# Performance work log

Hardware: AMD Instinct MI355X
Metric: run time of the kernel (lower is better)

## Reference

```python
import jax, jax.numpy as jnp
import numpy as np

D_MODEL = 1024
N_HEADS = 16
HEAD_DIM = D_MODEL // N_HEADS
SEQ_LEN = 2048
D_FF = 4 * D_MODEL
LCC_SCALE = 0.1
LN_EPS = 1e-5
NORM_EPS = 1e-12  # F.normalize eps


def _layer_norm(x, g, b):
    mu = jnp.mean(x, axis=-1, keepdims=True)
    var = jnp.mean(jnp.square(x - mu), axis=-1, keepdims=True)
    return (x - mu) * jax.lax.rsqrt(var + LN_EPS) * g + b


def setup_inputs() -> dict:
    key = jax.random.key(0)
    ks = jax.random.split(key, 8)
    s = 0.02  # weight init scale
    return {
        "x": jax.random.normal(ks[0], (SEQ_LEN, D_MODEL), jnp.float32),
        "lcc_values": jax.random.uniform(ks[1], (SEQ_LEN,), jnp.float32),
        "w_qkv": jax.random.normal(ks[2], (D_MODEL, 3 * D_MODEL), jnp.float32) * s,
        "b_qkv": jnp.zeros((3 * D_MODEL,), jnp.float32),
        "w_out": jax.random.normal(ks[3], (D_MODEL, D_MODEL), jnp.float32) * s,
        "b_out": jnp.zeros((D_MODEL,), jnp.float32),
        "ln1_g": jnp.ones((D_MODEL,), jnp.float32),
        "ln1_b": jnp.zeros((D_MODEL,), jnp.float32),
        "ln2_g": jnp.ones((D_MODEL,), jnp.float32),
        "ln2_b": jnp.zeros((D_MODEL,), jnp.float32),
        "w_ff1": jax.random.normal(ks[4], (D_MODEL, D_FF), jnp.float32) * s,
        "b_ff1": jnp.zeros((D_FF,), jnp.float32),
        "w_ff2": jax.random.normal(ks[5], (D_FF, D_MODEL), jnp.float32) * s,
        "b_ff2": jnp.zeros((D_MODEL,), jnp.float32),
    }


def reference(x, lcc_values, w_qkv, b_qkv, w_out, b_out, ln1_g, ln1_b,
              ln2_g, ln2_b, w_ff1, b_ff1, w_ff2, b_ff2):
    L = x.shape[0]
    scaling = HEAD_DIM ** -0.5

    normed = _layer_norm(x, ln1_g, ln1_b)
    qkv = normed @ w_qkv + b_qkv                      # [L, 3D]
    qkv = qkv.reshape(L, 3, N_HEADS, HEAD_DIM)
    q = jnp.transpose(qkv[:, 0], (1, 0, 2))           # [H, L, d]
    k = jnp.transpose(qkv[:, 1], (1, 0, 2))
    v = jnp.transpose(qkv[:, 2], (1, 0, 2))

    # cosine attention: L2-normalize q, k
    q = q / jnp.maximum(jnp.linalg.norm(q, axis=-1, keepdims=True), NORM_EPS)
    k = k / jnp.maximum(jnp.linalg.norm(k, axis=-1, keepdims=True), NORM_EPS)
    q = q * scaling

    scores = jnp.einsum('hld,hmd->hlm', q, k)         # [H, L, L]
    bias = (lcc_values[:, None] + lcc_values[None, :]) * 0.5 * LCC_SCALE
    scores = jnp.clip(scores + bias[None], -10.0, 10.0)
    probs = jax.nn.softmax(scores, axis=-1)

    attn = jnp.einsum('hlm,hmd->hld', probs, v)       # [H, L, d]
    attn = jnp.transpose(attn, (1, 0, 2)).reshape(L, D_MODEL)
    x = x + (attn @ w_out + b_out)

    normed2 = _layer_norm(x, ln2_g, ln2_b)
    h = jax.nn.gelu(normed2 @ w_ff1 + b_ff1, approximate=False)
    x = x + (h @ w_ff2 + b_ff2)
    return x
```

## Files before the change

### kernel.cpp

```cpp
#include <hip/hip_runtime.h>
#include <hip/hip_bf16.h>

#define D_MODEL 1024
#define SEQ 2048
#define NH 16
#define HD 64
#define DFF 4096

typedef __attribute__((ext_vector_type(8))) __bf16 bf16x8;
typedef __attribute__((ext_vector_type(4))) float f32x4;

__device__ __forceinline__ unsigned short f2bf(float f) {
    union { float f; unsigned u; } v; v.f = f;
    unsigned r = v.u + 0x7fffu + ((v.u >> 16) & 1u);
    return (unsigned short)(r >> 16);
}
__device__ __forceinline__ unsigned pack2(float a, float b) {
    return (unsigned)f2bf(a) | ((unsigned)f2bf(b) << 16);
}
__device__ __forceinline__ float bf2f(unsigned short u) {
    union { unsigned u; float f; } v; v.u = ((unsigned)u) << 16;
    return v.f;
}
__device__ __forceinline__ bf16x8 ld_frag(const unsigned short* p) {
    union { uint4 u; bf16x8 b; } c;
    c.u = *(const uint4*)p;
    return c.b;
}

typedef __attribute__((address_space(3))) unsigned lds_u32;
typedef const __attribute__((address_space(1))) unsigned glob_u32;
__device__ __forceinline__ void gl_lds16(const unsigned short* g, unsigned short* l) {
    __builtin_amdgcn_global_load_lds((glob_u32*)g, (lds_u32*)l, 16, 0, 0);
}

#define MFMA16(a,b,c) __builtin_amdgcn_mfma_f32_16x16x32_bf16(a,b,c,0,0,0)

__global__ __launch_bounds__(256) void wcast_all(const float* __restrict__ wq, const float* __restrict__ wo,
                                                 const float* __restrict__ wf1, const float* __restrict__ wf2,
                                                 unsigned short* __restrict__ oq, unsigned short* __restrict__ oo,
                                                 unsigned short* __restrict__ of1, unsigned short* __restrict__ of2) {
    __shared__ unsigned short lt[64][72];
    int id = blockIdx.x;
    const float* W; unsigned short* O; int K, N, nb, kb;
    if (id < 768)       { W = wq;  O = oq;  K = 1024; N = 3072; nb = id % 48; kb = id / 48; }
    else if (id < 1024) { id -= 768;  W = wo;  O = oo;  K = 1024; N = 1024; nb = id & 15; kb = id >> 4; }
    else if (id < 2048) { id -= 1024; W = wf1; O = of1; K = 1024; N = 4096; nb = id & 63; kb = id >> 6; }
    else                { id -= 2048; W = wf2; O = of2; K = 4096; N = 1024; nb = id & 15; kb = id >> 4; }
    int t = threadIdx.x;
    int r = t >> 2, c0 = (t & 3) << 4;
    const float* src = W + (size_t)(kb*64 + r) * N + nb*64 + c0;
    float4 f0 = ((const float4*)src)[0];
    float4 f1 = ((const float4*)src)[1];
    float4 f2 = ((const float4*)src)[2];
    float4 f3 = ((const float4*)src)[3];
    unsigned* dst = (unsigned*)&lt[r][c0];
    dst[0]=pack2(f0.x,f0.y); dst[1]=pack2(f0.z,f0.w);
    dst[2]=pack2(f1.x,f1.y); dst[3]=pack2(f1.z,f1.w);
    dst[4]=pack2(f2.x,f2.y); dst[5]=pack2(f2.z,f2.w);
    dst[6]=pack2(f3.x,f3.y); dst[7]=pack2(f3.z,f3.w);
    __syncthreads();
    int n_ = t >> 2, k0 = (t & 3) << 4;
    unsigned obuf[8];
#pragma unroll
    for (int i = 0; i < 8; i++)
        obuf[i] = (unsigned)lt[k0 + 2*i][n_] | ((unsigned)lt[k0 + 2*i + 1][n_] << 16);
    unsigned short* out = O + (size_t)(nb*64 + n_) * K + kb*64 + k0;
    ((uint4*)out)[0] = *(uint4*)&obuf[0];
    ((uint4*)out)[1] = *(uint4*)&obuf[4];
}

__global__ __launch_bounds__(256) void ln_kernel(const float* __restrict__ x,
                                                 const float* __restrict__ g,
                                                 const float* __restrict__ b,
                                                 unsigned short* __restrict__ out) {
    int row = blockIdx.x, t = threadIdx.x;
    float4 v = ((const float4*)(x + (size_t)row * D_MODEL))[t];
    float s  = v.x + v.y + v.z + v.w;
    float sq = v.x*v.x + v.y*v.y + v.z*v.z + v.w*v.w;
#pragma unroll
    for (int m = 1; m < 64; m <<= 1) { s += __shfl_xor(s, m, 64); sq += __shfl_xor(sq, m, 64); }
    __shared__ float ls[4], lq[4];
    int wave = t >> 6, lane = t & 63;
    if (lane == 0) { ls[wave] = s; lq[wave] = sq; }
    __syncthreads();
    s  = ls[0]+ls[1]+ls[2]+ls[3];
    sq = lq[0]+lq[1]+lq[2]+lq[3];
    float mu  = s * (1.0f / D_MODEL);
    float var = sq * (1.0f / D_MODEL) - mu * mu;
    float rs  = rsqrtf(var + 1e-5f);
    int c = t * 4;
    float y0 = (v.x - mu) * rs * g[c+0] + b[c+0];
    float y1 = (v.y - mu) * rs * g[c+1] + b[c+1];
    float y2 = (v.z - mu) * rs * g[c+2] + b[c+2];
    float y3 = (v.w - mu) * rs * g[c+3] + b[c+3];
    unsigned* o = (unsigned*)(out + (size_t)row * D_MODEL + c);
    o[0] = pack2(y0, y1); o[1] = pack2(y2, y3);
}

__global__ __launch_bounds__(256) void reduce_ln(const float* __restrict__ x,
                                                 const float* __restrict__ bout,
                                                 const unsigned short* __restrict__ parts,
                                                 const float* __restrict__ g,
                                                 const float* __restrict__ b,
                                                 float* __restrict__ x1,
                                                 unsigned short* __restrict__ x2n) {
    int row = blockIdx.x, t = threadIdx.x;
    int i = row * 256 + t;
    float4 v = ((const float4*)x)[i];
    float4 bb = ((const float4*)bout)[t];
    v.x += bb.x; v.y += bb.y; v.z += bb.z; v.w += bb.w;
    ushort4 u0 = ((const ushort4*)parts)[i];
    ushort4 u1 = ((const ushort4*)(parts + (size_t)SEQ*D_MODEL))[i];
    v.x += bf2f(u0.x) + bf2f(u1.x);
    v.y += bf2f(u0.y) + bf2f(u1.y);
    v.z += bf2f(u0.z) + bf2f(u1.z);
    v.w += bf2f(u0.w) + bf2f(u1.w);
    ((float4*)x1)[i] = v;
    float s  = v.x + v.y + v.z + v.w;
    float sq = v.x*v.x + v.y*v.y + v.z*v.z + v.w*v.w;
#pragma unroll
    for (int m = 1; m < 64; m <<= 1) { s += __shfl_xor(s, m, 64); sq += __shfl_xor(sq, m, 64); }
    __shared__ float ls[4], lq[4];
    int wave = t >> 6, lane = t & 63;
    if (lane == 0) { ls[wave] = s; lq[wave] = sq; }
    __syncthreads();
    s  = ls[0]+ls[1]+ls[2]+ls[3];
    sq = lq[0]+lq[1]+lq[2]+lq[3];
    float mu  = s * (1.0f / D_MODEL);
    float var = sq * (1.0f / D_MODEL) - mu * mu;
    float rs  = rsqrtf(var + 1e-5f);
    int c = t * 4;
    float y0 = (v.x - mu) * rs * g[c+0] + b[c+0];
    float y1 = (v.y - mu) * rs * g[c+1] + b[c+1];
    float y2 = (v.z - mu) * rs * g[c+2] + b[c+2];
    float y3 = (v.w - mu) * rs * g[c+3] + b[c+3];
    unsigned* o = (unsigned*)(x2n + (size_t)row * D_MODEL + c);
    o[0] = pack2(y0, y1); o[1] = pack2(y2, y3);
}

__global__ __launch_bounds__(256) void reduce_ff2(const float* __restrict__ res,
                                                  const float* __restrict__ bias,
                                                  const unsigned short* __restrict__ parts,
                                                  float* __restrict__ out) {
    int i = blockIdx.x * 256 + threadIdx.x;
    float4 r = ((const float4*)res)[i];
    float4 b = ((const float4*)bias)[i & (D_MODEL/4 - 1)];
    r.x += b.x; r.y += b.y; r.z += b.z; r.w += b.w;
#pragma unroll
    for (int p = 0; p < 4; p++) {
        ushort4 u = ((const ushort4*)(parts + (size_t)p * SEQ * D_MODEL))[i];
        r.x += bf2f(u.x); r.y += bf2f(u.y); r.z += bf2f(u.z); r.w += bf2f(u.w);
    }
    ((float4*)out)[i] = r;
}

#define TMg 128
#define TNg 128
#define BKq 32
#define BUF_U16 ((TMg + TNg) * BKq)
#define SMEM_U16 (4 * BUF_U16)
__device__ __forceinline__ void gemm_core(const unsigned short* __restrict__ A,
                                          const unsigned short* __restrict__ Bt,
                                          int K, int K0, int KS, int bm, int bn,
                                          unsigned short* smem, f32x4 acc[4][4],
                                          int wave, int lane) {
    int quad = lane >> 4, lr = lane & 15;
    const unsigned short* pa[2]; const unsigned short* pb[2];
    int aoff[2], boff[2];
#pragma unroll
    for (int i = 0; i < 2; i++) {
        int rl = i*64 + wave*16 + (lane >> 2);
        int sc = (lane & 3) ^ (rl & 3);
        pa[i] = A + (size_t)(bm*TMg + rl) * K + K0 + sc*8;
        pb[i] = Bt + (size_t)(bn*TNg + rl) * K + K0 + sc*8;
        aoff[i] = (i*64 + wave*16) * BKq;
        boff[i] = TMg*BKq + (i*64 + wave*16) * BKq;
    }
    int wr = (wave >> 1) * 64, wc = (wave & 1) * 64;
    int foA[4], foB[4];
#pragma unroll
    for (int i = 0; i < 4; i++) {
        int ra = wr + i*16 + lr;
        foA[i] = ra*BKq + (quad ^ (ra & 3))*8;
        int rb = wc + i*16 + lr;
        foB[i] = TMg*BKq + rb*BKq + (quad ^ (rb & 3))*8;
    }
    int T = KS >> 5;
#pragma unroll
    for (int t = 0; t < 3; t++) {
        unsigned short* s = smem + t * BUF_U16;
#pragma unroll
        for (int i = 0; i < 2; i++) {
            gl_lds16(pa[i] + t*BKq, s + aoff[i]);
            gl_lds16(pb[i] + t*BKq, s + boff[i]);
        }
    }
    for (int t = 0; t < T; t++) {
        if (t < T - 2)      asm volatile("s_waitcnt vmcnt(8)" ::: "memory");
        else if (t == T - 2) asm volatile("s_waitcnt vmcnt(4)" ::: "memory");
        else                 asm volatile("s_waitcnt vmcnt(0)" ::: "memory");
        __builtin_amdgcn_s_barrier();
        if (t + 3 < T) {
            unsigned short* s = smem + ((t + 3) & 3) * BUF_U16;
#pragma unroll
            for (int i = 0; i < 2; i++) {
                gl_lds16(pa[i] + (t+3)*BKq, s + aoff[i]);
                gl_lds16(pb[i] + (t+3)*BKq, s + boff[i]);
            }
        }
        const unsigned short* s = smem + (t & 3) * BUF_U16;
        bf16x8 af[4], bfr[4];
#pragma unroll
        for (int i = 0; i < 4; i++) af[i] = ld_frag(s + foA[i]);
#pragma unroll
        for (int j = 0; j < 4; j++) bfr[j] = ld_frag(s + foB[j]);
        __builtin_amdgcn_s_setprio(1);
#pragma unroll
        for (int i = 0; i < 4; i++)
#pragma unroll
            for (int j = 0; j < 4; j++)
                acc[i][j] = MFMA16(af[i], bfr[j], acc[i][j]);
        __builtin_amdgcn_s_setprio(0);
    }
}

__device__ __forceinline__ void acc_init(f32x4 acc[4][4]) {
    f32x4 z = {0.f, 0.f, 0.f, 0.f};
#pragma unroll
    for (int i = 0; i < 4; i++)
#pragma unroll
        for (int j = 0; j < 4; j++) acc[i][j] = z;
}

__global__ __launch_bounds__(256) void k_gemm_qkv(const unsigned short* __restrict__ A,
                                                  const unsigned short* __restrict__ Bt,
                                                  const float* __restrict__ bias,
                                                  unsigned short* __restrict__ qn,
                                                  unsigned short* __restrict__ kn,
                                                  unsigned short* __restrict__ vt) {
    __shared__ unsigned short smem[SMEM_U16];
    int t = threadIdx.x;
    int bn = blockIdx.x, bm = blockIdx.y;
    int wave = t >> 6, lane = t & 63;
    int quad = lane >> 4, lr = lane & 15;
    f32x4 acc[4][4];
    acc_init(acc);
    gemm_core(A, Bt, 1024, 0, 1024, bm, bn, smem, acc, wave, lane);

    int wr = (wave >> 1) * 64, wc = (wave & 1) * 64;
    int sec = bn >> 3, hp = bn & 7;
    float bv[4];
#pragma unroll
    for (int j = 0; j < 4; j++) bv[j] = bias[bn*TNg + wc + j*16 + lr];
#pragma unroll
    for (int i = 0; i < 4; i++)
#pragma unroll
        for (int j = 0; j < 4; j++)
#pragma unroll
            for (int r = 0; r < 4; r++) acc[i][j][r] += bv[j];

    if (sec < 2) {
        int h = hp*2 + (wave & 1);
        unsigned short* dst = (sec == 0) ? qn : kn;
        float mul = (sec == 0) ? 0.125f : 1.0f;
#pragma unroll
        for (int i = 0; i < 4; i++)
#pragma unroll
            for (int r = 0; r < 4; r++) {
                float ss = 0.f;
#pragma unroll
                for (int j = 0; j < 4; j++) ss += acc[i][j][r]*acc[i][j][r];
                ss += __shfl_xor(ss, 1, 64); ss += __shfl_xor(ss, 2, 64);
                ss += __shfl_xor(ss, 4, 64); ss += __shfl_xor(ss, 8, 64);
                float scale = mul / fmaxf(sqrtf(ss), 1e-12f);
                int row = bm*TMg + wr + i*16 + quad*4 + r;
                size_t base = ((size_t)h*SEQ + row) * HD;
#pragma unroll
                for (int j = 0; j < 4; j++)
                    dst[base + j*16 + lr] = f2bf(acc[i][j][r] * scale);
            }
    } else {
        __syncthreads();
        unsigned short (*lv)[136] = (unsigned short (*)[136])smem;
#pragma unroll
        for (int i = 0; i < 4; i++)
#pragma unroll
            for (int j = 0; j < 4; j++)
#pragma unroll
                for (int r = 0; r < 4; r++)
                    lv[wc + j*16 + lr][wr + i*16 + quad*4 + r] = f2bf(acc[i][j][r]);
        __syncthreads();
        int d = t >> 1, l0 = (t & 1) * 64;
        unsigned short* ov = vt + ((size_t)(hp*128 + d)) * SEQ + bm*TMg + l0;
#pragma unroll
        for (int c = 0; c < 8; c++)
            ((uint4*)ov)[c] = *(uint4*)&lv[d][l0 + c*8];
    }
}

template<int SPLITK>
__device__ __forceinline__ void gemm_part(const unsigned short* A, const unsigned short* Bt,
                                          unsigned short* C, int M, int N, int K) {
    __shared__ unsigned short smem[SMEM_U16];
    int t = threadIdx.x;
    int bn = blockIdx.x, bm = blockIdx.y, kz = blockIdx.z;
    int wave = t >> 6, lane = t & 63;
    int quad = lane >> 4, lr = lane & 15;
    int KS = K / SPLITK;
    f32x4 acc[4][4];
    acc_init(acc);
    gemm_core(A, Bt, K, kz*KS, KS, bm, bn, smem, acc, wave, lane);
    int wr = (wave >> 1) * 64, wc = (wave & 1) * 64;
    unsigned short* P = C + (size_t)kz * M * N;
#pragma unroll
    for (int i = 0; i < 4; i++)
#pragma unroll
        for (int j = 0; j < 4; j++) {
            int row0 = bm*TMg + wr + i*16 + quad*4;
            int col  = bn*TNg + wc + j*16 + lr;
#pragma unroll
            for (int r = 0; r < 4; r++)
                P[(size_t)(row0 + r) * N + col] = f2bf(acc[i][j][r]);
        }
}
__global__ __launch_bounds__(256) void k_gemm_op(const unsigned short* A, const unsigned short* Bt,
                                                 unsigned short* C, int M, int N, int K) {
    gemm_part<2>(A, Bt, C, M, N, K);
}
__global__ __launch_bounds__(256) void k_gemm_ff2(const unsigned short* A, const unsigned short* Bt,
                                                  unsigned short* C, int M, int N, int K) {
    gemm_part<4>(A, Bt, C, M, N, K);
}

__global__ __launch_bounds__(256) void k_gemm_ff1(const unsigned short* __restrict__ A,
                                                  const unsigned short* __restrict__ Bt,
                                                  const float* __restrict__ bias,
                                                  unsigned short* __restrict__ C,
                                                  int M, int N, int K) {
    __shared__ unsigned short smem[SMEM_U16];
    int t = threadIdx.x;
    int bn = blockIdx.x, bm = blockIdx.y;
    int wave = t >> 6, lane = t & 63;
    int quad = lane >> 4, lr = lane & 15;
    f32x4 acc[4][4];
    acc_init(acc);
    gemm_core(A, Bt, K, 0, K, bm, bn, smem, acc, wave, lane);
    int wr = (wave >> 1) * 64, wc = (wave & 1) * 64;
#pragma unroll
    for (int i = 0; i < 4; i++)
#pragma unroll
        for (int j = 0; j < 4; j++) {
            int row0 = bm*TMg + wr + i*16 + quad*4;
            int col  = bn*TNg + wc + j*16 + lr;
            float bvv = bias[col];
#pragma unroll
            for (int r = 0; r < 4; r++) {
                float v = acc[i][j][r] + bvv;
                v = 0.5f * v * (1.0f + erff(v * 0.70710678118654752f));
                C[(size_t)(row0 + r) * N + col] = f2bf(v);
            }
        }
}

#define KSPLIT 2
#define KTILES (SEQ / 64 / KSPLIT)
__global__ __launch_bounds__(256) void attn_kernel(const unsigned short* __restrict__ qn,
                                                   const unsigned short* __restrict__ kn,
                                                   const unsigned short* __restrict__ vt,
                                                   const float* __restrict__ lcc,
                                                   float* __restrict__ num_ws,
                                                   float* __restrict__ den_ws) {
    __shared__ unsigned short lQP[64*64];
    __shared__ unsigned short lK[2][64*64];
    __shared__ unsigned short lV[2][64*64];
    int h = blockIdx.x, qb = blockIdx.y, kz = blockIdx.z;
    int t = threadIdx.x;
    int wave = t >> 6, lane = t & 63, quad = lane >> 4, lr = lane & 15;
    int r0 = lane >> 3;
    int ch = lane & 7;

    const unsigned short* kn0 = kn + (size_t)h*SEQ*HD + (size_t)kz*(SEQ/KSPLIT)*HD;
    const unsigned short* vt0 = vt + (size_t)h*HD*SEQ + kz*(SEQ/KSPLIT);
    const float* lcc0 = lcc + kz*(SEQ/KSPLIT);

#pragma unroll
    for (int i = 0; i < 2; i++) {
        int rl = wave*16 + i*8 + r0;
        int ss = ch ^ (rl & 7);
        gl_lds16(qn + ((size_t)h*SEQ + qb*64 + rl)*HD + ss*8, lQP + (wave*16 + i*8)*64);
        gl_lds16(kn0 + (size_t)rl*HD + ss*8,                  lK[0] + (wave*16 + i*8)*64);
        gl_lds16(vt0 + (size_t)rl*SEQ + ss*8,                 lV[0] + (wave*16 + i*8)*64);
    }
    __syncthreads();

    bf16x8 aq0 = ld_frag(lQP + (wave*16 + lr)*64 + ((quad     ^ (lr & 7)))*8);
    bf16x8 aq1 = ld_frag(lQP + (wave*16 + lr)*64 + (((quad+4) ^ (lr & 7)))*8);

    f32x4 z = {0.f, 0.f, 0.f, 0.f};
    f32x4 oacc[4]; oacc[0]=z; oacc[1]=z; oacc[2]=z; oacc[3]=z;
    float den[4] = {0.f, 0.f, 0.f, 0.f};

    int cur = 0;
    for (int kb = 0; kb < KTILES; kb++) {
        if (kb + 1 < KTILES) {
            int nxt = cur ^ 1;
#pragma unroll
            for (int i = 0; i < 2; i++) {
                int rl = wave*16 + i*8 + r0;
                int ss = ch ^ (rl & 7);
                gl_lds16(kn0 + (size_t)(kb+1)*64*HD + (size_t)rl*HD + ss*8,
                         lK[nxt] + (wave*16 + i*8)*64);
                gl_lds16(vt0 + (size_t)rl*SEQ + (kb+1)*64 + ss*8,
                         lV[nxt] + (wave*16 + i*8)*64);
            }
        }
        float lmv[4];
#pragma unroll
        for (int j = 0; j < 4; j++) lmv[j] = 0.05f * lcc0[kb*64 + j*16 + lr];

        __builtin_amdgcn_s_setprio(1);
        const unsigned short* Kc = lK[cur];
#pragma unroll
        for (int j = 0; j < 4; j++) {
            bf16x8 b0 = ld_frag(Kc + (j*16 + lr)*64 + ((quad     ^ (lr & 7)))*8);
            bf16x8 b1 = ld_frag(Kc + (j*16 + lr)*64 + (((quad+4) ^ (lr & 7)))*8);
            f32x4 s = z;
            s = MFMA16(aq0, b0, s);
            s = MFMA16(aq1, b1, s);
#pragma unroll
            for (int r = 0; r < 4; r++) {
                float p = __expf(s[r] + lmv[j]);
                den[r] += p;
                int prow = wave*16 + quad*4 + r;
                lQP[prow*64 + (((2*j + (lr >> 3)) ^ (prow & 7)))*8 + (lr & 7)] = f2bf(p);
            }
        }
        bf16x8 ap0 = ld_frag(lQP + (wave*16 + lr)*64 + ((quad     ^ (lr & 7)))*8);
        bf16x8 ap1 = ld_frag(lQP + (wave*16 + lr)*64 + (((quad+4) ^ (lr & 7)))*8);
        const unsigned short* Vc = lV[cur];
#pragma unroll
        for (int j2 = 0; j2 < 4; j2++) {
            bf16x8 b0 = ld_frag(Vc + (j2*16 + lr)*64 + ((quad     ^ (lr & 7)))*8);
            bf16x8 b1 = ld_frag(Vc + (j2*16 + lr)*64 + (((quad+4) ^ (lr & 7)))*8);
            oacc[j2] = MFMA16(ap0, b0, oacc[j2]);
            oacc[j2] = MFMA16(ap1, b1, oacc[j2]);
        }
        __builtin_amdgcn_s_setprio(0);
        __syncthreads();
        cur ^= 1;
    }
#pragma unroll
    for (int r = 0; r < 4; r++)
#pragma unroll
        for (int m = 1; m < 16; m <<= 1) den[r] += __shfl_xor(den[r], m, 64);

    float* nump = num_ws + (((size_t)(h*32 + qb)) * KSPLIT + kz) * 4096;
#pragma unroll
    for (int j2 = 0; j2 < 4; j2++)
#pragma unroll
        for (int r = 0; r < 4; r++)
            nump[(wave*16 + quad*4 + r) * 64 + j2*16 + lr] = oacc[j2][r];
    if (lr == 0) {
        float* denp = den_ws + (((size_t)(h*32 + qb)) * KSPLIT + kz) * 64;
#pragma unroll
        for (int r = 0; r < 4; r++) denp[wave*16 + quad*4 + r] = den[r];
    }
}

__global__ __launch_bounds__(256) void attn_comb(const float* __restrict__ num_ws,
                                                 const float* __restrict__ den_ws,
                                                 unsigned short* __restrict__ attn) {
    int hq = blockIdx.x;
    int h = hq >> 5, qb = hq & 31;
    int t = threadIdx.x;
    int row = t >> 2, col0 = (t & 3) << 4;
    const float* n0 = num_ws + ((size_t)hq * KSPLIT) * 4096 + row*64 + col0;
    const float* n1 = n0 + 4096;
    float d = den_ws[(size_t)hq * KSPLIT * 64 + row] + den_ws[((size_t)hq * KSPLIT + 1) * 64 + row];
    float inv = 1.0f / d;
    unsigned ob[8];
#pragma unroll
    for (int i = 0; i < 4; i++) {
        float4 a = ((const float4*)n0)[i];
        float4 b = ((const float4*)n1)[i];
        ob[2*i]   = pack2((a.x + b.x) * inv, (a.y + b.y) * inv);
        ob[2*i+1] = pack2((a.z + b.z) * inv, (a.w + b.w) * inv);
    }
    unsigned short* op = attn + (size_t)(qb*64 + row) * D_MODEL + h*64 + col0;
    ((uint4*)op)[0] = *(uint4*)&ob[0];
    ((uint4*)op)[1] = *(uint4*)&ob[4];
}

extern "C" void kernel_launch(void* const* d_in, const int* in_sizes, int n_in,
                              void* d_out, int out_size, void* d_ws, size_t ws_size,
                              hipStream_t stream) {
    const float* x      = (const float*)d_in[0];
    const float* lcc    = (const float*)d_in[1];
    const float* w_qkv  = (const float*)d_in[2];
    const float* b_qkv  = (const float*)d_in[3];
    const float* w_out  = (const float*)d_in[4];
    const float* b_out  = (const float*)d_in[5];
    const float* ln1_g  = (const float*)d_in[6];
    const float* ln1_b  = (const float*)d_in[7];
    const float* ln2_g  = (const float*)d_in[8];
    const float* ln2_b  = (const float*)d_in[9];
    const float* w_ff1  = (const float*)d_in[10];
    const float* b_ff1  = (const float*)d_in[11];
    const float* w_ff2  = (const float*)d_in[12];
    const float* b_ff2  = (const float*)d_in[13];

    char* ws = (char*)d_ws;
    unsigned short* wtq  = (unsigned short*)(ws);
    unsigned short* wto  = (unsigned short*)(ws + 6291456);
    unsigned short* wtf1 = (unsigned short*)(ws + 8388608);
    unsigned short* wtf2 = (unsigned short*)(ws + 16777216);
    unsigned short* xn   = (unsigned short*)(ws + 25165824);
    float*          x1   = (float*)(ws + 29360128);
    float*          numw = (float*)(ws + 29360128);
    float*          denw = (float*)(ws + 46137344);
    unsigned short* hbuf = (unsigned short*)(ws + 37748736);
    unsigned short* pOP  = (unsigned short*)(ws + 37748736);
    unsigned short* qnb  = (unsigned short*)(ws + 54525952);
    unsigned short* knb  = (unsigned short*)(ws + 58720256);
    unsigned short* vtb  = (unsigned short*)(ws + 62914560);
    unsigned short* pFF2 = (unsigned short*)(ws);
    unsigned short* attnb = xn;
    unsigned short* x2n  = qnb;
    float* outp = (float*)d_out;


    wcast_all<<<3072, 256, 0, stream>>>(w_qkv, w_out, w_ff1, w_ff2, wtq, wto, wtf1, wtf2);
    ln_kernel<<<SEQ, 256, 0, stream>>>(x, ln1_g, ln1_b, xn);
    k_gemm_qkv<<<dim3(24, 16), 256, 0, stream>>>(xn, wtq, b_qkv, qnb, knb, vtb);
    attn_kernel<<<dim3(16, 32, KSPLIT), 256, 0, stream>>>(qnb, knb, vtb, lcc, numw, denw);
    attn_comb<<<512, 256, 0, stream>>>(numw, denw, attnb);
    k_gemm_op<<<dim3(8, 16, 2), 256, 0, stream>>>(attnb, wto, pOP, SEQ, 1024, 1024);
    reduce_ln<<<SEQ, 256, 0, stream>>>(x, b_out, pOP, ln2_g, ln2_b, x1, x2n);
    k_gemm_ff1<<<dim3(32, 16), 256, 0, stream>>>(x2n, wtf1, b_ff1, hbuf, SEQ, 4096, 1024);
    k_gemm_ff2<<<dim3(8, 16, 4), 256, 0, stream>>>(hbuf, wtf2, pFF2, SEQ, 1024, 4096);
    reduce_ff2<<<SEQ*D_MODEL/1024, 256, 0, stream>>>(x1, b_ff2, pFF2, outp);
}
```

Baseline: 269.4 us.

## Switch GEMMs to 512-thread blocks with intra-block K-split and BK=64

The GEMM core now uses 8 waves per 128x128 tile. Two wave groups each take half of a 64-wide K slice, and their accumulators are merged through shared memory. The old 4-stage BK=32 pipeline becomes a 2-stage BK=64 double buffer with an 8-way swizzle. The out-projection split-K rises from 2 to 4, with reduce_ln updated to sum four partials. The aim is more waves per tile to hide latency and fewer barriers, at the cost of the LDS merge, extra syncs and a shallower prefetch.

New measurement: 994.1 us. 3.69x slower.

```diff
diff --git a/kernel.cpp b/kernel.cpp
--- a/kernel.cpp
+++ b/kernel.cpp
@@ -110,12 +110,11 @@
     float4 v = ((const float4*)x)[i];
     float4 bb = ((const float4*)bout)[t];
     v.x += bb.x; v.y += bb.y; v.z += bb.z; v.w += bb.w;
-    ushort4 u0 = ((const ushort4*)parts)[i];
-    ushort4 u1 = ((const ushort4*)(parts + (size_t)SEQ*D_MODEL))[i];
-    v.x += bf2f(u0.x) + bf2f(u1.x);
-    v.y += bf2f(u0.y) + bf2f(u1.y);
-    v.z += bf2f(u0.z) + bf2f(u1.z);
-    v.w += bf2f(u0.w) + bf2f(u1.w);
+#pragma unroll
+    for (int p = 0; p < 4; p++) {
+        ushort4 u = ((const ushort4*)(parts + (size_t)p * SEQ * D_MODEL))[i];
+        v.x += bf2f(u.x); v.y += bf2f(u.y); v.z += bf2f(u.z); v.w += bf2f(u.w);
+    }
     ((float4*)x1)[i] = v;
     float s  = v.x + v.y + v.z + v.w;
     float sq = v.x*v.x + v.y*v.y + v.z*v.z + v.w*v.w;
@@ -157,59 +156,50 @@
 
 #define TMg 128
 #define TNg 128
-#define BKq 32
-#define BUF_U16 ((TMg + TNg) * BKq)
-#define SMEM_U16 (4 * BUF_U16)
-__device__ __forceinline__ void gemm_core(const unsigned short* __restrict__ A,
-                                          const unsigned short* __restrict__ Bt,
-                                          int K, int K0, int KS, int bm, int bn,
-                                          unsigned short* smem, f32x4 acc[4][4],
-                                          int wave, int lane) {
+#define HALFg ((TMg + TNg) * 64)
+#define SMEM_U16 (2 * HALFg)
+__device__ __forceinline__ void gemm_core512(const unsigned short* __restrict__ A,
+                                             const unsigned short* __restrict__ Bt,
+                                             int K, int K0, int KS, int bm, int bn,
+                                             unsigned short* smem, f32x4 acc[4][4],
+                                             int w, int lane) {
     int quad = lane >> 4, lr = lane & 15;
+    int kg = w >> 2;
     const unsigned short* pa[2]; const unsigned short* pb[2];
     int aoff[2], boff[2];
 #pragma unroll
     for (int i = 0; i < 2; i++) {
-        int rl = i*64 + wave*16 + (lane >> 2);
-        int sc = (lane & 3) ^ (rl & 3);
-        pa[i] = A + (size_t)(bm*TMg + rl) * K + K0 + sc*8;
+        int rl = i*64 + w*8 + (lane >> 3);
+        int sc = (lane & 7) ^ (rl & 7);
+        pa[i] = A  + (size_t)(bm*TMg + rl) * K + K0 + sc*8;
         pb[i] = Bt + (size_t)(bn*TNg + rl) * K + K0 + sc*8;
-        aoff[i] = (i*64 + wave*16) * BKq;
-        boff[i] = TMg*BKq + (i*64 + wave*16) * BKq;
-    }
-    int wr = (wave >> 1) * 64, wc = (wave & 1) * 64;
+        aoff[i] = (i*64 + w*8) * 64;
+        boff[i] = TMg*64 + (i*64 + w*8) * 64;
+    }
+    int wr = ((w >> 1) & 1) * 64, wc = (w & 1) * 64;
     int foA[4], foB[4];
 #pragma unroll
     for (int i = 0; i < 4; i++) {
         int ra = wr + i*16 + lr;
-        foA[i] = ra*BKq + (quad ^ (ra & 3))*8;
+        foA[i] = ra*64 + (((quad + 4*kg) ^ (ra & 7)))*8;
         int rb = wc + i*16 + lr;
-        foB[i] = TMg*BKq + rb*BKq + (quad ^ (rb & 3))*8;
-    }
-    int T = KS >> 5;
-#pragma unroll
-    for (int t = 0; t < 3; t++) {
-        unsigned short* s = smem + t * BUF_U16;
-#pragma unroll
-        for (int i = 0; i < 2; i++) {
-            gl_lds16(pa[i] + t*BKq, s + aoff[i]);
-            gl_lds16(pb[i] + t*BKq, s + boff[i]);
-        }
-    }
+        foB[i] = TMg*64 + rb*64 + (((quad + 4*kg) ^ (rb & 7)))*8;
+    }
+#pragma unroll
+    for (int i = 0; i < 2; i++) { gl_lds16(pa[i], smem + aoff[i]); gl_lds16(pb[i], smem + boff[i]); }
+    int bo = 0;
+    int T = KS >> 6;
     for (int t = 0; t < T; t++) {
-        if (t < T - 2)      asm volatile("s_waitcnt vmcnt(8)" ::: "memory");
-        else if (t == T - 2) asm volatile("s_waitcnt vmcnt(4)" ::: "memory");
-        else                 asm volatile("s_waitcnt vmcnt(0)" ::: "memory");
-        __builtin_amdgcn_s_barrier();
-        if (t + 3 < T) {
-            unsigned short* s = smem + ((t + 3) & 3) * BUF_U16;
+        __syncthreads();
+        if (t + 1 < T) {
+            int nb = bo ^ HALFg;
 #pragma unroll
             for (int i = 0; i < 2; i++) {
-                gl_lds16(pa[i] + (t+3)*BKq, s + aoff[i]);
-                gl_lds16(pb[i] + (t+3)*BKq, s + boff[i]);
+                gl_lds16(pa[i] + (t+1)*64, smem + nb + aoff[i]);
+                gl_lds16(pb[i] + (t+1)*64, smem + nb + boff[i]);
             }
         }
-        const unsigned short* s = smem + (t & 3) * BUF_U16;
+        const unsigned short* s = smem + bo;
         bf16x8 af[4], bfr[4];
 #pragma unroll
         for (int i = 0; i < 4; i++) af[i] = ld_frag(s + foA[i]);
@@ -222,6 +212,7 @@
             for (int j = 0; j < 4; j++)
                 acc[i][j] = MFMA16(af[i], bfr[j], acc[i][j]);
         __builtin_amdgcn_s_setprio(0);
+        bo ^= HALFg;
     }
 }
 
@@ -233,124 +224,179 @@
         for (int j = 0; j < 4; j++) acc[i][j] = z;
 }
 
-__global__ __launch_bounds__(256) void k_gemm_qkv(const unsigned short* __restrict__ A,
-                                                  const unsigned short* __restrict__ Bt,
-                                                  const float* __restrict__ bias,
-                                                  unsigned short* __restrict__ qn,
-                                                  unsigned short* __restrict__ kn,
-                                                  unsigned short* __restrict__ vt) {
+__device__ __forceinline__ void acc_merge_split(unsigned short* smem, f32x4 acc[4][4],
+                                                int w, int lane) {
+    float* X = (float*)smem;
+    int kg = w >> 2, p = w & 3, quad = lane >> 4, lr = lane & 15;
+    __syncthreads();
+#pragma unroll
+    for (int jj = 0; jj < 2; jj++) {
+        int j = (kg ^ 1)*2 + jj;
+        float* slot = X + (p*4 + j)*1024;
+#pragma unroll
+        for (int i = 0; i < 4; i++)
+#pragma unroll
+            for (int r = 0; r < 4; r++)
+                slot[(i*16 + r*4 + quad)*16 + lr] = acc[i][j][r];
+    }
+    __syncthreads();
+#pragma unroll
+    for (int jj = 0; jj < 2; jj++) {
+        int j = kg*2 + jj;
+        const float* slot = X + (p*4 + j)*1024;
+#pragma unroll
+        for (int i = 0; i < 4; i++)
+#pragma unroll
+            for (int r = 0; r < 4; r++)
+                acc[i][j][r] += slot[(i*16 + r*4 + quad)*16 + lr];
+    }
+}
+
+__global__ __launch_bounds__(512, 4) void k_gemm_qkv(const unsigned short* __restrict__ A,
+                                                     const unsigned short* __restrict__ Bt,
+                                                     const float* __restrict__ bias,
+                                                     unsigned short* __restrict__ qn,
+                                                     unsigned short* __restrict__ kn,
+                                                     unsigned short* __restrict__ vt) {
     __shared__ unsigned short smem[SMEM_U16];
     int t = threadIdx.x;
     int bn = blockIdx.x, bm = blockIdx.y;
-    int wave = t >> 6, lane = t & 63;
+    int w = t >> 6, lane = t & 63;
     int quad = lane >> 4, lr = lane & 15;
     f32x4 acc[4][4];
     acc_init(acc);
-    gemm_core(A, Bt, 1024, 0, 1024, bm, bn, smem, acc, wave, lane);
-
-    int wr = (wave >> 1) * 64, wc = (wave & 1) * 64;
+    gemm_core512(A, Bt, 1024, 0, 1024, bm, bn, smem, acc, w, lane);
+
+    float* X = (float*)smem;
+    int kg = w >> 2, p = w & 3;
+    __syncthreads();
+    if (kg == 1) {
+#pragma unroll
+        for (int j = 0; j < 4; j++) {
+            float* slot = X + (p*4 + j)*1024;
+#pragma unroll
+            for (int i = 0; i < 4; i++)
+#pragma unroll
+                for (int r = 0; r < 4; r++)
+                    slot[(i*16 + r*4 + quad)*16 + lr] = acc[i][j][r];
+        }
+    }
+    __syncthreads();
+    int wr = ((w >> 1) & 1) * 64, wc = (w & 1) * 64;
     int sec = bn >> 3, hp = bn & 7;
-    float bv[4];
-#pragma unroll
-    for (int j = 0; j < 4; j++) bv[j] = bias[bn*TNg + wc + j*16 + lr];
-#pragma unroll
-    for (int i = 0; i < 4; i++)
-#pragma unroll
-        for (int j = 0; j < 4; j++)
-#pragma unroll
-            for (int r = 0; r < 4; r++) acc[i][j][r] += bv[j];
+    if (kg == 0) {
+#pragma unroll
+        for (int j = 0; j < 4; j++) {
+            const float* slot = X + (p*4 + j)*1024;
+            float bv = bias[bn*TNg + wc + j*16 + lr];
+#pragma unroll
+            for (int i = 0; i < 4; i++)
+#pragma unroll
+                for (int r = 0; r < 4; r++)
+                    acc[i][j][r] += slot[(i*16 + r*4 + quad)*16 + lr] + bv;
+        }
+    }
 
     if (sec < 2) {
-        int h = hp*2 + (wave & 1);
-        unsigned short* dst = (sec == 0) ? qn : kn;
-        float mul = (sec == 0) ? 0.125f : 1.0f;
-#pragma unroll
-        for (int i = 0; i < 4; i++)
-#pragma unroll
-            for (int r = 0; r < 4; r++) {
-                float ss = 0.f;
-#pragma unroll
-                for (int j = 0; j < 4; j++) ss += acc[i][j][r]*acc[i][j][r];
-                ss += __shfl_xor(ss, 1, 64); ss += __shfl_xor(ss, 2, 64);
-                ss += __shfl_xor(ss, 4, 64); ss += __shfl_xor(ss, 8, 64);
-                float scale = mul / fmaxf(sqrtf(ss), 1e-12f);
-                int row = bm*TMg + wr + i*16 + quad*4 + r;
-                size_t base = ((size_t)h*SEQ + row) * HD;
-#pragma unroll
-                for (int j = 0; j < 4; j++)
-                    dst[base + j*16 + lr] = f2bf(acc[i][j][r] * scale);
-            }
+        if (kg == 0) {
+            int h = hp*2 + (w & 1);
+            unsigned short* dst = (sec == 0) ? qn : kn;
+            float mul = (sec == 0) ? 0.125f : 1.0f;
+#pragma unroll
+            for (int i = 0; i < 4; i++)
+#pragma unroll
+                for (int r = 0; r < 4; r++) {
+                    float ss = 0.f;
+#pragma unroll
+                    for (int j = 0; j < 4; j++) ss += acc[i][j][r]*acc[i][j][r];
+                    ss += __shfl_xor(ss, 1, 64); ss += __shfl_xor(ss, 2, 64);
+                    ss += __shfl_xor(ss, 4, 64); ss += __shfl_xor(ss, 8, 64);
+                    float scale = mul / fmaxf(sqrtf(ss), 1e-12f);
+                    int row = bm*TMg + wr + i*16 + quad*4 + r;
+                    size_t base = ((size_t)h*SEQ + row) * HD;
+#pragma unroll
+                    for (int j = 0; j < 4; j++)
+                        dst[base + j*16 + lr] = f2bf(acc[i][j][r] * scale);
+                }
+        }
     } else {
         __syncthreads();
         unsigned short (*lv)[136] = (unsigned short (*)[136])smem;
-#pragma unroll
-        for (int i = 0; i < 4; i++)
-#pragma unroll
-            for (int j = 0; j < 4; j++)
-#pragma unroll
-                for (int r = 0; r < 4; r++)
-                    lv[wc + j*16 + lr][wr + i*16 + quad*4 + r] = f2bf(acc[i][j][r]);
+        if (kg == 0) {
+#pragma unroll
+            for (int i = 0; i < 4; i++)
+#pragma unroll
+                for (int j = 0; j < 4; j++)
+#pragma unroll
+                    for (int r = 0; r < 4; r++)
+                        lv[wc + j*16 + lr][wr + i*16 + quad*4 + r] = f2bf(acc[i][j][r]);
+        }
         __syncthreads();
-        int d = t >> 1, l0 = (t & 1) * 64;
+        int d = t >> 2, l0 = (t & 3) * 32;
         unsigned short* ov = vt + ((size_t)(hp*128 + d)) * SEQ + bm*TMg + l0;
 #pragma unroll
-        for (int c = 0; c < 8; c++)
+        for (int c = 0; c < 4; c++)
             ((uint4*)ov)[c] = *(uint4*)&lv[d][l0 + c*8];
     }
 }
 
 template<int SPLITK>
-__device__ __forceinline__ void gemm_part(const unsigned short* A, const unsigned short* Bt,
-                                          unsigned short* C, int M, int N, int K) {
+__device__ __forceinline__ void gemm_part512(const unsigned short* A, const unsigned short* Bt,
+                                             unsigned short* C, int M, int N, int K) {
     __shared__ unsigned short smem[SMEM_U16];
     int t = threadIdx.x;
     int bn = blockIdx.x, bm = blockIdx.y, kz = blockIdx.z;
-    int wave = t >> 6, lane = t & 63;
+    int w = t >> 6, lane = t & 63;
     int quad = lane >> 4, lr = lane & 15;
     int KS = K / SPLITK;
     f32x4 acc[4][4];
     acc_init(acc);
-    gemm_core(A, Bt, K, kz*KS, KS, bm, bn, smem, acc, wave, lane);
-    int wr = (wave >> 1) * 64, wc = (wave & 1) * 64;
+    gemm_core512(A, Bt, K, kz*KS, KS, bm, bn, smem, acc, w, lane);
+    acc_merge_split(smem, acc, w, lane);
+    int kg = w >> 2, wr = ((w >> 1) & 1) * 64, wc = (w & 1) * 64;
     unsigned short* P = C + (size_t)kz * M * N;
 #pragma unroll
-    for (int i = 0; i < 4; i++)
-#pragma unroll
-        for (int j = 0; j < 4; j++) {
+    for (int jj = 0; jj < 2; jj++) {
+        int j = kg*2 + jj;
+#pragma unroll
+        for (int i = 0; i < 4; i++) {
             int row0 = bm*TMg + wr + i*16 + quad*4;
             int col  = bn*TNg + wc + j*16 + lr;
 #pragma unroll
             for (int r = 0; r < 4; r++)
                 P[(size_t)(row0 + r) * N + col] = f2bf(acc[i][j][r]);
         }
-}
-__global__ __launch_bounds__(256) void k_gemm_op(const unsigned short* A, const unsigned short* Bt,
-                                                 unsigned short* C, int M, int N, int K) {
-    gemm_part<2>(A, Bt, C, M, N, K);
-}
-__global__ __launch_bounds__(256) void k_gemm_ff2(const unsigned short* A, const unsigned short* Bt,
-                                                  unsigned short* C, int M, int N, int K) {
-    gemm_part<4>(A, Bt, C, M, N, K);
-}
-
-__global__ __launch_bounds__(256) void k_gemm_ff1(const unsigned short* __restrict__ A,
-                                                  const unsigned short* __restrict__ Bt,
-                                                  const float* __restrict__ bias,
-                                                  unsigned short* __restrict__ C,
-                                                  int M, int N, int K) {
+    }
+}
+__global__ __launch_bounds__(512, 4) void k_gemm_op(const unsigned short* A, const unsigned short* Bt,
+                                                    unsigned short* C, int M, int N, int K) {
+    gemm_part512<4>(A, Bt, C, M, N, K);
+}
+__global__ __launch_bounds__(512, 4) void k_gemm_ff2(const unsigned short* A, const unsigned short* Bt,
+                                                     unsigned short* C, int M, int N, int K) {
+    gemm_part512<4>(A, Bt, C, M, N, K);
+}
+
+__global__ __launch_bounds__(512, 4) void k_gemm_ff1(const unsigned short* __restrict__ A,
+                                                     const unsigned short* __restrict__ Bt,
+                                                     const float* __restrict__ bias,
+                                                     unsigned short* __restrict__ C,
+                                                     int M, int N, int K) {
     __shared__ unsigned short smem[SMEM_U16];
     int t = threadIdx.x;
     int bn = blockIdx.x, bm = blockIdx.y;
-    int wave = t >> 6, lane = t & 63;
+    int w = t >> 6, lane = t & 63;
     int quad = lane >> 4, lr = lane & 15;
     f32x4 acc[4][4];
     acc_init(acc);
-    gemm_core(A, Bt, K, 0, K, bm, bn, smem, acc, wave, lane);
-    int wr = (wave >> 1) * 64, wc = (wave & 1) * 64;
-#pragma unroll
-    for (int i = 0; i < 4; i++)
-#pragma unroll
-        for (int j = 0; j < 4; j++) {
+    gemm_core512(A, Bt, K, 0, K, bm, bn, smem, acc, w, lane);
+    acc_merge_split(smem, acc, w, lane);
+    int kg = w >> 2, wr = ((w >> 1) & 1) * 64, wc = (w & 1) * 64;
+#pragma unroll
+    for (int jj = 0; jj < 2; jj++) {
+        int j = kg*2 + jj;
+#pragma unroll
+        for (int i = 0; i < 4; i++) {
             int row0 = bm*TMg + wr + i*16 + quad*4;
             int col  = bn*TNg + wc + j*16 + lr;
             float bvv = bias[col];
@@ -361,6 +407,7 @@
                 C[(size_t)(row0 + r) * N + col] = f2bf(v);
             }
         }
+    }
 }
 
 #define KSPLIT 2
@@ -532,12 +579,12 @@
 
     wcast_all<<<3072, 256, 0, stream>>>(w_qkv, w_out, w_ff1, w_ff2, wtq, wto, wtf1, wtf2);
     ln_kernel<<<SEQ, 256, 0, stream>>>(x, ln1_g, ln1_b, xn);
-    k_gemm_qkv<<<dim3(24, 16), 256, 0, stream>>>(xn, wtq, b_qkv, qnb, knb, vtb);
+    k_gemm_qkv<<<dim3(24, 16), 512, 0, stream>>>(xn, wtq, b_qkv, qnb, knb, vtb);
     attn_kernel<<<dim3(16, 32, KSPLIT), 256, 0, stream>>>(qnb, knb, vtb, lcc, numw, denw);
     attn_comb<<<512, 256, 0, stream>>>(numw, denw, attnb);
-    k_gemm_op<<<dim3(8, 16, 2), 256, 0, stream>>>(attnb, wto, pOP, SEQ, 1024, 1024);
+    k_gemm_op<<<dim3(8, 16, 4), 512, 0, stream>>>(attnb, wto, pOP, SEQ, 1024, 1024);
     reduce_ln<<<SEQ, 256, 0, stream>>>(x, b_out, pOP, ln2_g, ln2_b, x1, x2n);
-    k_gemm_ff1<<<dim3(32, 16), 256, 0, stream>>>(x2n, wtf1, b_ff1, hbuf, SEQ, 4096, 1024);
-    k_gemm_ff2<<<dim3(8, 16, 4), 256, 0, stream>>>(hbuf, wtf2, pFF2, SEQ, 1024, 4096);
+    k_gemm_ff1<<<dim3(32, 16), 512, 0, stream>>>(x2n, wtf1, b_ff1, hbuf, SEQ, 4096, 1024);
+    k_gemm_ff2<<<dim3(8, 16, 4), 512, 0, stream>>>(hbuf, wtf2, pFF2, SEQ, 1024, 4096);
     reduce_ff2<<<SEQ*D_MODEL/1024, 256, 0, stream>>>(x1, b_ff2, pFF2, outp);
 }
```
